# Performance work log

Hardware: AMD Instinct MI355X
Metric: run time of the kernel (lower is better)

The kernel has to match this reference:

```python
import jax, jax.numpy as jnp
import numpy as np

HEADS = 16
DIM_HEAD = 64


def setup_inputs() -> dict:
    key = jax.random.key(0)
    k1, k2, k3 = jax.random.split(key, 3)
    b, n, dim = 2, 2048, 1024
    x = jax.random.normal(k1, (b, n, dim), dtype=jnp.float32)
    W_qkv = jax.random.normal(k2, (dim, 6 * HEADS * DIM_HEAD), dtype=jnp.float32) * 0.02
    W_out = jax.random.normal(k3, (HEADS * DIM_HEAD, dim), dtype=jnp.float32) * 0.02
    return {"x": x, "W_qkv": W_qkv, "W_out": W_out}


def reference(x, W_qkv, W_out):
    b, n, _ = x.shape
    h, d = HEADS, DIM_HEAD
    scale = d ** -0.5

    # project and split into 6 head-wise tensors: (qkv h d) grouping order
    qkv = (x @ W_qkv).reshape(b, n, 6, h, d).transpose(2, 0, 3, 1, 4)  # [6,b,h,n,d]
    qu, ku, vu, qc, kc, vc = qkv
    qu_s = qu * scale
    qc_s = qc * scale

    idx = jnp.arange(n)
    future = idx[None, :] > idx[:, None]  # torch triu(1): True strictly above diag

    # term1: qc . vu, zeroed on future positions
    term1 = jnp.einsum('bhid,bhjd->bhij', qc_s, vu)
    term1 = jnp.where(future, 0.0, term1)

    # sigmoid lookahead attention, kept ONLY on strictly-future positions
    lookahead = jax.nn.sigmoid(jnp.einsum('bhid,bhjd->bhij', qu_s, ku))
    lookahead = jnp.where(future, lookahead, 0.0)

    # Su[i,k] = sum_j term1[i,j] * lookahead[k,j]
    Su = jnp.einsum('bhij,bhkj->bhik', term1, lookahead)
    Sc = jnp.einsum('bhid,bhjd->bhij', qc_s, kc)

    scores = Sc - jax.nn.silu(Su)
    neg = -jnp.finfo(scores.dtype).max
    scores = jnp.where(future, neg, scores)

    attn = jax.nn.softmax(scores, axis=-1)
    out = jnp.einsum('bhij,bhjd->bhid', attn, vc)  # [b,h,n,d]

    out = out.transpose(0, 2, 1, 3).reshape(b, n, h * d)
    return out @ W_out
```

## Files before the change

### kernel.cpp

```cpp
#include <hip/hip_runtime.h>
#include <hip/hip_bf16.h>
#include <stdint.h>


typedef unsigned short u16;
typedef __attribute__((ext_vector_type(8))) short s8v;
typedef __attribute__((ext_vector_type(4))) float f4v;

#define LDS_STRIDE 40

__device__ __forceinline__ u16 f2bf(float f) {
  union { float f; unsigned u; } v; v.f = f;
  unsigned r = v.u + 0x7FFFu + ((v.u >> 16) & 1u);
  return (u16)(r >> 16);
}
__device__ __forceinline__ float bf2f(u16 u) {
  union { unsigned u; float f; } v; v.u = ((unsigned)u) << 16; return v.f;
}

__device__ __forceinline__ int swz128(int r, int c) { return r * 128 + (c ^ ((r & 7) << 3)); }
__device__ __forceinline__ int swz64v(int r, int c) { return r * 64 + (c ^ ((r & 7) << 3)); }

typedef __attribute__((address_space(1))) const void* gas_t;
typedef __attribute__((address_space(3))) void* las_t;
__device__ __forceinline__ void gld16(const void* g, void* l) {
  __builtin_amdgcn_global_load_lds((gas_t)g, (las_t)l, 16, 0, 0);
}

__device__ __forceinline__ void stage_tile(u16* __restrict__ dst, const u16* __restrict__ src,
                                           int rows, long srcStride, int tid, int nthreads) {
  for (int i = tid; i < rows * 4; i += nthreads) {
    int r = i >> 2, seg = i & 3;
    *(uint4*)(&dst[r * LDS_STRIDE + seg * 8]) =
        *(const uint4*)(&src[(long)r * srcStride + seg * 8]);
  }
}

__device__ __forceinline__ void mfma_tile(const u16* As, const u16* Bs, int lane,
                                          int wm, int wn, f4v acc[4][4]) {
  const int rl = lane & 15;
  const int ks = (lane >> 4) * 8;
  s8v a[4], b[4];
#pragma unroll
  for (int m = 0; m < 4; ++m)
    a[m] = *(const s8v*)(&As[(wm * 64 + m * 16 + rl) * LDS_STRIDE + ks]);
#pragma unroll
  for (int n = 0; n < 4; ++n)
    b[n] = *(const s8v*)(&Bs[(wn * 64 + n * 16 + rl) * LDS_STRIDE + ks]);
#pragma unroll
  for (int m = 0; m < 4; ++m)
#pragma unroll
    for (int n = 0; n < 4; ++n)
      acc[m][n] = __builtin_amdgcn_mfma_f32_16x16x32_bf16(a[m], b[n], acc[m][n], 0, 0, 0);
}

__device__ __forceinline__ void zero_acc(f4v acc[4][4]) {
  f4v z = {0.f, 0.f, 0.f, 0.f};
#pragma unroll
  for (int m = 0; m < 4; ++m)
#pragma unroll
    for (int n = 0; n < 4; ++n) acc[m][n] = z;
}


__global__ void convert_x_kernel(const float* __restrict__ in, u16* __restrict__ out) {
  int i = (blockIdx.x * 256 + threadIdx.x) * 4;
  float4 v = *(const float4*)(&in[i]);
  out[i + 0] = f2bf(v.x);
  out[i + 1] = f2bf(v.y);
  out[i + 2] = f2bf(v.z);
  out[i + 3] = f2bf(v.w);
}

__global__ void transpose_convert_kernel(const float* __restrict__ in, u16* __restrict__ out,
                                         int R, int C) {
  __shared__ float tile[32][33];
  int c0 = blockIdx.x * 32, r0 = blockIdx.y * 32;
  for (int rr = threadIdx.y; rr < 32; rr += 8)
    tile[rr][threadIdx.x] = in[(size_t)(r0 + rr) * C + (c0 + threadIdx.x)];
  __syncthreads();
  for (int cc = threadIdx.y; cc < 32; cc += 8)
    out[(size_t)(c0 + cc) * R + (r0 + threadIdx.x)] = f2bf(tile[threadIdx.x][cc]);
}


__global__ __launch_bounds__(256) void gemm_qkv_kernel(
    const u16* __restrict__ xb, const u16* __restrict__ wqkvT,
    u16* __restrict__ quS, u16* __restrict__ ku, u16* __restrict__ vu,
    u16* __restrict__ qcS, u16* __restrict__ kc, u16* __restrict__ vcT) {
  __shared__ u16 As[128 * LDS_STRIDE], Bs[128 * LDS_STRIDE];
  int bm = blockIdx.x, bn = blockIdx.y;
  int tid = threadIdx.x, lane = tid & 63, w = tid >> 6, wm = w >> 1, wn = w & 1;
  f4v acc[4][4];
  zero_acc(acc);
  for (int kk = 0; kk < 1024; kk += 32) {
    stage_tile(As, xb + (size_t)(bm * 128) * 1024 + kk, 128, 1024, tid, 256);
    stage_tile(Bs, wqkvT + (size_t)(bn * 128) * 1024 + kk, 128, 1024, tid, 256);
    __syncthreads();
    mfma_tile(As, Bs, lane, wm, wn, acc);
    __syncthreads();
  }
#pragma unroll
  for (int m = 0; m < 4; ++m)
#pragma unroll
    for (int n = 0; n < 4; ++n)
#pragma unroll
      for (int j = 0; j < 4; ++j) {
        int row = bm * 128 + wm * 64 + m * 16 + ((lane >> 4) * 4) + j;
        int col = bn * 128 + wn * 64 + n * 16 + (lane & 15);
        float v = acc[m][n][j];
        int b = row >> 11, nn = row & 2047;
        int s = col >> 10, hh = (col >> 6) & 15, dd = col & 63;
        int bh = (b << 4) + hh;
        size_t idx = ((size_t)bh * 2048 + nn) * 64 + dd;
        switch (s) {
          case 0: quS[idx] = f2bf(v * 0.125f); break;
          case 1: ku[idx] = f2bf(v); break;
          case 2: vu[idx] = f2bf(v); break;
          case 3: qcS[idx] = f2bf(v * 0.125f); break;
          case 4: kc[idx] = f2bf(v); break;
          default: vcT[((size_t)bh * 64 + dd) * 2048 + nn] = f2bf(v); break;
        }
      }
}


__global__ __launch_bounds__(256) void tl_kernel(
    const u16* __restrict__ qcS, const u16* __restrict__ vu,
    const u16* __restrict__ quS, const u16* __restrict__ ku,
    u16* __restrict__ term1p, u16* __restrict__ lookp, int c0) {
  __shared__ u16 As[128 * LDS_STRIDE], Bs[128 * LDS_STRIDE];
  int t = blockIdx.x, lb = blockIdx.y, z = blockIdx.z;
  int bh = c0 + lb;
  int I = 0;
  while ((I + 1) * (I + 2) / 2 <= t) ++I;
  int K = t - I * (I + 1) / 2;
  int rt = z ? K : I;
  int ct = z ? I : K;
  const u16* A = (z ? quS : qcS) + ((size_t)bh * 2048 + rt * 128) * 64;
  const u16* B = (z ? ku : vu) + ((size_t)bh * 2048 + ct * 128) * 64;
  u16* o = (z ? lookp : term1p) + ((size_t)lb * 136 + t) * 16384;
  int tid = threadIdx.x, lane = tid & 63, w = tid >> 6, wm = w >> 1, wn = w & 1;
  f4v acc[4][4];
  zero_acc(acc);
  for (int kk = 0; kk < 64; kk += 32) {
    stage_tile(As, A + kk, 128, 64, tid, 256);
    stage_tile(Bs, B + kk, 128, 64, tid, 256);
    __syncthreads();
    mfma_tile(As, Bs, lane, wm, wn, acc);
    __syncthreads();
  }
#pragma unroll
  for (int m = 0; m < 4; ++m)
#pragma unroll
    for (int n = 0; n < 4; ++n)
#pragma unroll
      for (int j = 0; j < 4; ++j) {
        int lr = wm * 64 + m * 16 + ((lane >> 4) * 4) + j;
        int lc = wn * 64 + n * 16 + (lane & 15);
        int gr = rt * 128 + lr, gc = ct * 128 + lc;
        float v = acc[m][n][j];
        if (z)
          v = (gc > gr) ? 1.f / (1.f + __expf(-v)) : 0.f;
        else
          v = (gc > gr) ? 0.f : v;
        o[swz128(lr, lc)] = f2bf(v);
      }
}


__global__ __launch_bounds__(256, 2) void castle_kernel(
    const u16* __restrict__ term1p, const u16* __restrict__ lookp,
    const u16* __restrict__ qcS, const u16* __restrict__ kc,
    const u16* __restrict__ vcT,
    u16* __restrict__ opart, float* __restrict__ ml, int c0) {
  __shared__ u16 sA[16384];
  __shared__ u16 sB[16384];
  int sid = blockIdx.x, lb = blockIdx.y, bh = c0 + lb;
  int d = 15, acc0 = 0;
  while (acc0 + (16 - d) <= sid) { acc0 += 16 - d; --d; }
  int K = sid - acc0;
  int I = d + K;
  int t = I * (I + 1) / 2 + K;

  int tid = threadIdx.x, lane = tid & 63, w = tid >> 6;
  int g = lane >> 4, l15 = lane & 15;

  const u16* t1b = term1p + (size_t)lb * 136 * 16384;
  const u16* lkb = lookp + (size_t)lb * 136 * 16384;

  s8v qa[2][2];
#pragma unroll
  for (int mg = 0; mg < 2; ++mg)
#pragma unroll
    for (int kk = 0; kk < 2; ++kk)
      qa[mg][kk] = *(const s8v*)(&qcS[((size_t)bh * 2048 + I * 128 + w * 32 + mg * 16 + l15) * 64 +
                                      kk * 32 + g * 8]);

  f4v su[2][8];
  {
    f4v z = {0.f, 0.f, 0.f, 0.f};
#pragma unroll
    for (int mg = 0; mg < 2; ++mg)
#pragma unroll
      for (int n = 0; n < 8; ++n) su[mg][n] = z;
  }

  int bo = w * 1024 + (lane << 4);

  for (int j = K; j <= I; ++j) {
    __syncthreads();
    const char* srcA = (const char*)(t1b + (size_t)(I * (I + 1) / 2 + j) * 16384);
    const char* srcB = (const char*)(lkb + (size_t)(j * (j + 1) / 2 + K) * 16384);
#pragma unroll
    for (int it = 0; it < 8; ++it) {
      gld16(srcA + bo + it * 4096, (char*)sA + bo + it * 4096);
      gld16(srcB + bo + it * 4096, (char*)sB + bo + it * 4096);
    }
    __syncthreads();
#pragma unroll
    for (int kk = 0; kk < 4; ++kk) {
      s8v a[2], b[8];
      int c = kk * 32 + g * 8;
#pragma unroll
      for (int mg = 0; mg < 2; ++mg)
        a[mg] = *(const s8v*)(&sA[swz128(w * 32 + mg * 16 + l15, c)]);
#pragma unroll
      for (int n = 0; n < 8; ++n)
        b[n] = *(const s8v*)(&sB[swz128(n * 16 + l15, c)]);
#pragma unroll
      for (int mg = 0; mg < 2; ++mg)
#pragma unroll
        for (int n = 0; n < 8; ++n)
          su[mg][n] = __builtin_amdgcn_mfma_f32_16x16x32_bf16(a[mg], b[n], su[mg][n], 0, 0, 0);
    }
  }

  __syncthreads();
  {
#pragma unroll
    for (int it = 0; it < 4; ++it) {
      int o = bo + it * 4096;
      int row = o >> 7, lo = o & 127;
      const u16* src = kc + ((size_t)bh * 2048 + K * 128 + row) * 64 +
                       ((lo ^ ((row & 7) << 4)) >> 1);
      gld16(src, (char*)sB + o);
    }
#pragma unroll
    for (int it = 0; it < 4; ++it) {
      int o = bo + it * 4096;
      int rowd = o >> 8, lo = o & 255;
      const u16* src = vcT + ((size_t)bh * 64 + rowd) * 2048 + K * 128 +
                       ((lo ^ ((rowd & 7) << 4)) >> 1);
      gld16(src, (char*)sB + 16384 + o);
    }
  }
#pragma unroll
  for (int mg = 0; mg < 2; ++mg)
#pragma unroll
    for (int n = 0; n < 8; ++n)
#pragma unroll
      for (int j4 = 0; j4 < 4; ++j4) {
        float xv = su[mg][n][j4];
        su[mg][n][j4] = -(xv / (1.f + __expf(-xv)));
      }
  __syncthreads();

#pragma unroll
  for (int kk = 0; kk < 2; ++kk) {
    s8v b[8];
    int c = kk * 32 + g * 8;
#pragma unroll
    for (int n = 0; n < 8; ++n)
      b[n] = *(const s8v*)(&sB[swz64v(n * 16 + l15, c)]);
#pragma unroll
    for (int mg = 0; mg < 2; ++mg)
#pragma unroll
      for (int n = 0; n < 8; ++n)
        su[mg][n] = __builtin_amdgcn_mfma_f32_16x16x32_bf16(qa[mg][kk], b[n], su[mg][n], 0, 0, 0);
  }

  if (K == I) {
#pragma unroll
    for (int mg = 0; mg < 2; ++mg)
#pragma unroll
      for (int n = 0; n < 8; ++n)
#pragma unroll
        for (int j4 = 0; j4 < 4; ++j4) {
          int lr = w * 32 + mg * 16 + g * 4 + j4;
          int lc = n * 16 + l15;
          if (lc > lr) su[mg][n][j4] = -3.0e38f;
        }
  }

  float mrow[2][4], lrow[2][4];
#pragma unroll
  for (int mg = 0; mg < 2; ++mg)
#pragma unroll
    for (int j4 = 0; j4 < 4; ++j4) {
      float v = -3.0e38f;
#pragma unroll
      for (int n = 0; n < 8; ++n) v = fmaxf(v, su[mg][n][j4]);
      v = fmaxf(v, __shfl_xor(v, 1));
      v = fmaxf(v, __shfl_xor(v, 2));
      v = fmaxf(v, __shfl_xor(v, 4));
      v = fmaxf(v, __shfl_xor(v, 8));
      mrow[mg][j4] = v;
    }
  __syncthreads();
#pragma unroll
  for (int mg = 0; mg < 2; ++mg)
#pragma unroll
    for (int j4 = 0; j4 < 4; ++j4) {
      float sum = 0.f;
      int prow = w * 32 + mg * 16 + g * 4 + j4;
#pragma unroll
      for (int n = 0; n < 8; ++n) {
        float e = __expf(su[mg][n][j4] - mrow[mg][j4]);
        sum += e;
        sA[swz128(prow, n * 16 + l15)] = f2bf(e);
      }
      sum += __shfl_xor(sum, 1);
      sum += __shfl_xor(sum, 2);
      sum += __shfl_xor(sum, 4);
      sum += __shfl_xor(sum, 8);
      lrow[mg][j4] = sum;
    }
  __syncthreads();

  f4v o[2][4];
  {
    f4v z = {0.f, 0.f, 0.f, 0.f};
#pragma unroll
    for (int mg = 0; mg < 2; ++mg)
#pragma unroll
      for (int nd = 0; nd < 4; ++nd) o[mg][nd] = z;
  }
#pragma unroll
  for (int kk = 0; kk < 4; ++kk) {
    s8v pa[2], vb[4];
    int c = kk * 32 + g * 8;
#pragma unroll
    for (int mg = 0; mg < 2; ++mg)
      pa[mg] = *(const s8v*)(&sA[swz128(w * 32 + mg * 16 + l15, c)]);
#pragma unroll
    for (int nd = 0; nd < 4; ++nd)
      vb[nd] = *(const s8v*)(&sB[8192 + swz128(nd * 16 + l15, c)]);
#pragma unroll
    for (int mg = 0; mg < 2; ++mg)
#pragma unroll
      for (int nd = 0; nd < 4; ++nd)
        o[mg][nd] = __builtin_amdgcn_mfma_f32_16x16x32_bf16(pa[mg], vb[nd], o[mg][nd], 0, 0, 0);
  }

  size_t tb = (size_t)lb * 136 + t;
#pragma unroll
  for (int mg = 0; mg < 2; ++mg)
#pragma unroll
    for (int nd = 0; nd < 4; ++nd)
#pragma unroll
      for (int j4 = 0; j4 < 4; ++j4) {
        int prow = w * 32 + mg * 16 + g * 4 + j4;
        int dcol = nd * 16 + l15;
        opart[(tb * 128 + prow) * 64 + dcol] = f2bf(o[mg][nd][j4]);
      }
  if (l15 == 0) {
#pragma unroll
    for (int mg = 0; mg < 2; ++mg)
#pragma unroll
      for (int j4 = 0; j4 < 4; ++j4) {
        int prow = w * 32 + mg * 16 + g * 4 + j4;
        ml[tb * 256 + prow] = mrow[mg][j4];
        ml[tb * 256 + 128 + prow] = lrow[mg][j4];
      }
  }
}


__global__ __launch_bounds__(256) void combine_kernel(const u16* __restrict__ opart,
                                                      const float* __restrict__ ml,
                                                      u16* __restrict__ attn, int c0) {
  int lb = blockIdx.x, I = blockIdx.y, bh = c0 + lb;
  int tid = threadIdx.x;
  int row = tid >> 1, dh = (tid & 1) << 5;
  float M = -3.0e38f, L = 0.f;
  float O[32];
#pragma unroll
  for (int i = 0; i < 32; ++i) O[i] = 0.f;
  for (int K = 0; K <= I; ++K) {
    size_t tb = (size_t)lb * 136 + I * (I + 1) / 2 + K;
    float m = ml[tb * 256 + row];
    float l = ml[tb * 256 + 128 + row];
    float newM = fmaxf(M, m);
    float so = __expf(M - newM), sn = __expf(m - newM);
    L = L * so + l * sn;
    const u16* op = opart + (tb * 128 + row) * 64 + dh;
#pragma unroll
    for (int q = 0; q < 4; ++q) {
      s8v ov = *(const s8v*)(op + q * 8);
#pragma unroll
      for (int e = 0; e < 8; ++e)
        O[q * 8 + e] = O[q * 8 + e] * so + bf2f((u16)ov[e]) * sn;
    }
    M = newM;
  }
  float inv = 1.f / L;
  int b = bh >> 4, hh = bh & 15;
  u16* dst = attn + ((size_t)b * 2048 + I * 128 + row) * 1024 + hh * 64 + dh;
#pragma unroll
  for (int i = 0; i < 32; ++i) dst[i] = f2bf(O[i] * inv);
}


__global__ __launch_bounds__(256) void gemm_out_kernel(const u16* __restrict__ attn,
                                                       const u16* __restrict__ woutT,
                                                       float* __restrict__ out) {
  __shared__ u16 As[128 * LDS_STRIDE], Bs[128 * LDS_STRIDE];
  int bm = blockIdx.x, bn = blockIdx.y;
  int tid = threadIdx.x, lane = tid & 63, w = tid >> 6, wm = w >> 1, wn = w & 1;
  f4v acc[4][4];
  zero_acc(acc);
  for (int kk = 0; kk < 1024; kk += 32) {
    stage_tile(As, attn + (size_t)(bm * 128) * 1024 + kk, 128, 1024, tid, 256);
    stage_tile(Bs, woutT + (size_t)(bn * 128) * 1024 + kk, 128, 1024, tid, 256);
    __syncthreads();
    mfma_tile(As, Bs, lane, wm, wn, acc);
    __syncthreads();
  }
#pragma unroll
  for (int m = 0; m < 4; ++m)
#pragma unroll
    for (int n = 0; n < 4; ++n)
#pragma unroll
      for (int j = 0; j < 4; ++j) {
        int row = bm * 128 + wm * 64 + m * 16 + ((lane >> 4) * 4) + j;
        int col = bn * 128 + wn * 64 + n * 16 + (lane & 15);
        out[(size_t)row * 1024 + col] = acc[m][n][j];
      }
}


extern "C" void kernel_launch(void* const* d_in, const int* in_sizes, int n_in,
                              void* d_out, int out_size, void* d_ws, size_t ws_size,
                              hipStream_t stream) {
  const float* x = (const float*)d_in[0];
  const float* Wqkv = (const float*)d_in[1];
  const float* Wout = (const float*)d_in[2];
  float* out = (float*)d_out;

  char* base = (char*)d_ws;
  size_t off = 0;
  auto alloc = [&](size_t bytes) -> void* {
    void* p = base + off;
    off += (bytes + 255) & ~(size_t)255;
    return p;
  };

  u16* woutT = (u16*)alloc(1024ull * 1024 * 2);
  u16* quS = (u16*)alloc(32ull * 2048 * 64 * 2);
  u16* ku = (u16*)alloc(32ull * 2048 * 64 * 2);
  u16* vu = (u16*)alloc(32ull * 2048 * 64 * 2);
  u16* qcS = (u16*)alloc(32ull * 2048 * 64 * 2);
  u16* kc = (u16*)alloc(32ull * 2048 * 64 * 2);
  u16* vcT = (u16*)alloc(32ull * 2048 * 64 * 2);
  u16* attn = (u16*)alloc(4096ull * 1024 * 2);

  size_t perBH = 136ull * 16384 * 2 * 2 + 136ull * 128 * 64 * 2 + 136ull * 256 * 4;
  size_t remain = (ws_size > off) ? (ws_size - off) : 0;
  int chunk = (int)(remain / perBH);
  if (chunk < 1) chunk = 1;
  if (chunk > 32) chunk = 32;
  u16* term1p = (u16*)alloc((size_t)chunk * 136 * 16384 * 2);
  u16* lookp = (u16*)alloc((size_t)chunk * 136 * 16384 * 2);
  u16* opart = (u16*)alloc((size_t)chunk * 136 * 8192 * 2);
  float* mlb = (float*)alloc((size_t)chunk * 136 * 256 * 4);

  u16* xb = term1p;
  u16* wqkvT = term1p + 4096ull * 1024;

  convert_x_kernel<<<4096, 256, 0, stream>>>(x, xb);
  transpose_convert_kernel<<<dim3(192, 32), dim3(32, 8), 0, stream>>>(Wqkv, wqkvT, 1024, 6144);
  transpose_convert_kernel<<<dim3(32, 32), dim3(32, 8), 0, stream>>>(Wout, woutT, 1024, 1024);
  gemm_qkv_kernel<<<dim3(32, 48), 256, 0, stream>>>(xb, wqkvT, quS, ku, vu, qcS, kc, vcT);

  for (int c0 = 0; c0 < 32; c0 += chunk) {
    int nb = (32 - c0 < chunk) ? (32 - c0) : chunk;
    tl_kernel<<<dim3(136, nb, 2), 256, 0, stream>>>(qcS, vu, quS, ku, term1p, lookp, c0);
    castle_kernel<<<dim3(136, nb), 256, 0, stream>>>(term1p, lookp, qcS, kc, vcT, opart, mlb, c0);
    combine_kernel<<<dim3(nb, 16), 256, 0, stream>>>(opart, mlb, attn, c0);
  }
  gemm_out_kernel<<<dim3(32, 8), 256, 0, stream>>>(attn, woutT, out);
}
```

Measured before the change: 560.7 us.

## Stage GEMM epilogues through LDS for coalesced stores; add separate V transpose

The QKV GEMM and tl_kernel epilogues now write accumulators into shared memory in two passes, then issue 16-byte coalesced global stores instead of scattered 2-byte stores. The vc transpose moves out of the GEMM epilogue into a new transpose_v_kernel, which costs an extra launch and an extra buffer. The chunk cap drops from 32 to 16 heads, which means more passes over the tl, castle and combine kernels. The castle_kernel tile-index decode is also rewritten in a simpler form.

```diff
diff --git a/kernel.cpp b/kernel.cpp
--- a/kernel.cpp
+++ b/kernel.cpp
@@ -87,10 +87,13 @@
 __global__ __launch_bounds__(256) void gemm_qkv_kernel(
     const u16* __restrict__ xb, const u16* __restrict__ wqkvT,
     u16* __restrict__ quS, u16* __restrict__ ku, u16* __restrict__ vu,
-    u16* __restrict__ qcS, u16* __restrict__ kc, u16* __restrict__ vcT) {
-  __shared__ u16 As[128 * LDS_STRIDE], Bs[128 * LDS_STRIDE];
+    u16* __restrict__ qcS, u16* __restrict__ kc, u16* __restrict__ vcN) {
+  __shared__ u16 sh[10240];
+  u16* As = sh;
+  u16* Bs = sh + 5120;
   int bm = blockIdx.x, bn = blockIdx.y;
   int tid = threadIdx.x, lane = tid & 63, w = tid >> 6, wm = w >> 1, wn = w & 1;
+  int g = lane >> 4, l15 = lane & 15;
   f4v acc[4][4];
   zero_acc(acc);
   for (int kk = 0; kk < 1024; kk += 32) {
@@ -100,28 +103,65 @@
     mfma_tile(As, Bs, lane, wm, wn, acc);
     __syncthreads();
   }
-#pragma unroll
-  for (int m = 0; m < 4; ++m)
-#pragma unroll
-    for (int n = 0; n < 4; ++n)
-#pragma unroll
-      for (int j = 0; j < 4; ++j) {
-        int row = bm * 128 + wm * 64 + m * 16 + ((lane >> 4) * 4) + j;
-        int col = bn * 128 + wn * 64 + n * 16 + (lane & 15);
-        float v = acc[m][n][j];
-        int b = row >> 11, nn = row & 2047;
-        int s = col >> 10, hh = (col >> 6) & 15, dd = col & 63;
-        int bh = (b << 4) + hh;
-        size_t idx = ((size_t)bh * 2048 + nn) * 64 + dd;
-        switch (s) {
-          case 0: quS[idx] = f2bf(v * 0.125f); break;
-          case 1: ku[idx] = f2bf(v); break;
-          case 2: vu[idx] = f2bf(v); break;
-          case 3: qcS[idx] = f2bf(v * 0.125f); break;
-          case 4: kc[idx] = f2bf(v); break;
-          default: vcT[((size_t)bh * 64 + dd) * 2048 + nn] = f2bf(v); break;
-        }
-      }
+  int s = bn >> 3;
+  int b = bm >> 4;
+  int nn0 = (bm & 15) * 128;
+  int hh0 = (bn & 7) * 2;
+  float scale = (s == 0 || s == 3) ? 0.125f : 1.f;
+  u16* obase;
+  switch (s) {
+    case 0: obase = quS; break;
+    case 1: obase = ku; break;
+    case 2: obase = vu; break;
+    case 3: obase = qcS; break;
+    case 4: obase = kc; break;
+    default: obase = vcN; break;
+  }
+#pragma unroll
+  for (int pass = 0; pass < 2; ++pass) {
+    __syncthreads();
+    if (wn == pass) {
+#pragma unroll
+      for (int m = 0; m < 4; ++m)
+#pragma unroll
+        for (int n = 0; n < 4; ++n)
+#pragma unroll
+          for (int j = 0; j < 4; ++j) {
+            int lrow = wm * 64 + m * 16 + g * 4 + j;
+            int d = n * 16 + l15;
+            sh[lrow * 64 + d] = f2bf(acc[m][n][j] * scale);
+          }
+    }
+    __syncthreads();
+    int bh = (b << 4) + hh0 + pass;
+    u16* dst = obase + ((size_t)bh * 2048 + nn0) * 64;
+    for (int it = 0; it < 4; ++it) {
+      int e = (tid + it * 256) * 8;
+      *(uint4*)(dst + e) = *(const uint4*)(&sh[e]);
+    }
+  }
+}
+
+
+__global__ __launch_bounds__(256) void transpose_v_kernel(const u16* __restrict__ vcN,
+                                                          u16* __restrict__ vcT) {
+  __shared__ u16 t[64][72];
+  int nt = blockIdx.x, bh = blockIdx.y;
+  const u16* src = vcN + ((size_t)bh * 2048 + nt * 64) * 64;
+  int tid = threadIdx.x;
+  for (int i = tid; i < 512; i += 256) {
+    int r = i >> 3, cseg = i & 7;
+    *(uint4*)(&t[r][cseg * 8]) = *(const uint4*)(src + r * 64 + cseg * 8);
+  }
+  __syncthreads();
+  u16* dst = vcT + (size_t)bh * 64 * 2048 + nt * 64;
+  for (int i = tid; i < 512; i += 256) {
+    int d = i >> 3, nseg = i & 7;
+    u16 tmp[8];
+#pragma unroll
+    for (int e = 0; e < 8; ++e) tmp[e] = t[nseg * 8 + e][d];
+    *(uint4*)(dst + (size_t)d * 2048 + nseg * 8) = *(uint4*)tmp;
+  }
 }
 
 
@@ -129,7 +169,9 @@
     const u16* __restrict__ qcS, const u16* __restrict__ vu,
     const u16* __restrict__ quS, const u16* __restrict__ ku,
     u16* __restrict__ term1p, u16* __restrict__ lookp, int c0) {
-  __shared__ u16 As[128 * LDS_STRIDE], Bs[128 * LDS_STRIDE];
+  __shared__ u16 sh[10240];
+  u16* As = sh;
+  u16* Bs = sh + 5120;
   int t = blockIdx.x, lb = blockIdx.y, z = blockIdx.z;
   int bh = c0 + lb;
   int I = 0;
@@ -141,6 +183,7 @@
   const u16* B = (z ? ku : vu) + ((size_t)bh * 2048 + ct * 128) * 64;
   u16* o = (z ? lookp : term1p) + ((size_t)lb * 136 + t) * 16384;
   int tid = threadIdx.x, lane = tid & 63, w = tid >> 6, wm = w >> 1, wn = w & 1;
+  int g = lane >> 4, l15 = lane & 15;
   f4v acc[4][4];
   zero_acc(acc);
   for (int kk = 0; kk < 64; kk += 32) {
@@ -151,21 +194,33 @@
     __syncthreads();
   }
 #pragma unroll
-  for (int m = 0; m < 4; ++m)
-#pragma unroll
-    for (int n = 0; n < 4; ++n)
-#pragma unroll
-      for (int j = 0; j < 4; ++j) {
-        int lr = wm * 64 + m * 16 + ((lane >> 4) * 4) + j;
-        int lc = wn * 64 + n * 16 + (lane & 15);
-        int gr = rt * 128 + lr, gc = ct * 128 + lc;
-        float v = acc[m][n][j];
-        if (z)
-          v = (gc > gr) ? 1.f / (1.f + __expf(-v)) : 0.f;
-        else
-          v = (gc > gr) ? 0.f : v;
-        o[swz128(lr, lc)] = f2bf(v);
-      }
+  for (int pass = 0; pass < 2; ++pass) {
+    __syncthreads();
+    if (wm == pass) {
+#pragma unroll
+      for (int m = 0; m < 4; ++m)
+#pragma unroll
+        for (int n = 0; n < 4; ++n)
+#pragma unroll
+          for (int j = 0; j < 4; ++j) {
+            int lrl = m * 16 + g * 4 + j;
+            int lc = wn * 64 + n * 16 + l15;
+            int gr = rt * 128 + pass * 64 + lrl;
+            int gc = ct * 128 + lc;
+            float v = acc[m][n][j];
+            if (z)
+              v = (gc > gr) ? 1.f / (1.f + __expf(-v)) : 0.f;
+            else
+              v = (gc > gr) ? 0.f : v;
+            sh[lrl * 128 + (lc ^ ((lrl & 7) << 3))] = f2bf(v);
+          }
+    }
+    __syncthreads();
+    for (int it = 0; it < 4; ++it) {
+      int e = (tid + it * 256) * 8;
+      *(uint4*)(o + pass * 8192 + e) = *(const uint4*)(&sh[e]);
+    }
+  }
 }
 
 
@@ -177,10 +232,9 @@
   __shared__ u16 sA[16384];
   __shared__ u16 sB[16384];
   int sid = blockIdx.x, lb = blockIdx.y, bh = c0 + lb;
-  int d = 15, acc0 = 0;
-  while (acc0 + (16 - d) <= sid) { acc0 += 16 - d; --d; }
-  int K = sid - acc0;
-  int I = d + K;
+  int I = 15, rem = sid;
+  while (rem > I) { rem -= I + 1; --I; }
+  int K = rem;
   int t = I * (I + 1) / 2 + K;
 
   int tid = threadIdx.x, lane = tid & 63, w = tid >> 6;
@@ -415,7 +469,9 @@
 __global__ __launch_bounds__(256) void gemm_out_kernel(const u16* __restrict__ attn,
                                                        const u16* __restrict__ woutT,
                                                        float* __restrict__ out) {
-  __shared__ u16 As[128 * LDS_STRIDE], Bs[128 * LDS_STRIDE];
+  __shared__ u16 sh[10240];
+  u16* As = sh;
+  u16* Bs = sh + 5120;
   int bm = blockIdx.x, bn = blockIdx.y;
   int tid = threadIdx.x, lane = tid & 63, w = tid >> 6, wm = w >> 1, wn = w & 1;
   f4v acc[4][4];
@@ -462,6 +518,7 @@
   u16* vu = (u16*)alloc(32ull * 2048 * 64 * 2);
   u16* qcS = (u16*)alloc(32ull * 2048 * 64 * 2);
   u16* kc = (u16*)alloc(32ull * 2048 * 64 * 2);
+  u16* vcN = (u16*)alloc(32ull * 2048 * 64 * 2);
   u16* vcT = (u16*)alloc(32ull * 2048 * 64 * 2);
   u16* attn = (u16*)alloc(4096ull * 1024 * 2);
 
@@ -469,19 +526,27 @@
   size_t remain = (ws_size > off) ? (ws_size - off) : 0;
   int chunk = (int)(remain / perBH);
   if (chunk < 1) chunk = 1;
-  if (chunk > 32) chunk = 32;
+  if (chunk > 16) chunk = 16;
   u16* term1p = (u16*)alloc((size_t)chunk * 136 * 16384 * 2);
   u16* lookp = (u16*)alloc((size_t)chunk * 136 * 16384 * 2);
   u16* opart = (u16*)alloc((size_t)chunk * 136 * 8192 * 2);
   float* mlb = (float*)alloc((size_t)chunk * 136 * 256 * 4);
 
-  u16* xb = term1p;
-  u16* wqkvT = term1p + 4096ull * 1024;
+  u16* xb;
+  u16* wqkvT;
+  if ((size_t)chunk * 136 * 16384 * 2 >= (4096ull + 6144ull) * 1024 * 2) {
+    xb = term1p;
+    wqkvT = term1p + 4096ull * 1024;
+  } else {
+    xb = (u16*)alloc(4096ull * 1024 * 2);
+    wqkvT = (u16*)alloc(6144ull * 1024 * 2);
+  }
 
   convert_x_kernel<<<4096, 256, 0, stream>>>(x, xb);
   transpose_convert_kernel<<<dim3(192, 32), dim3(32, 8), 0, stream>>>(Wqkv, wqkvT, 1024, 6144);
   transpose_convert_kernel<<<dim3(32, 32), dim3(32, 8), 0, stream>>>(Wout, woutT, 1024, 1024);
-  gemm_qkv_kernel<<<dim3(32, 48), 256, 0, stream>>>(xb, wqkvT, quS, ku, vu, qcS, kc, vcT);
+  gemm_qkv_kernel<<<dim3(32, 48), 256, 0, stream>>>(xb, wqkvT, quS, ku, vu, qcS, kc, vcN);
+  transpose_v_kernel<<<dim3(32, 32), 256, 0, stream>>>(vcN, vcT);
 
   for (int c0 = 0; c0 < 32; c0 += chunk) {
     int nb = (32 - c0 < chunk) ? (32 - c0) : chunk;
```

Measured after the change: 657.8 us. +17.3%, slower.
